# Kernel tuning notes

Hardware: AMD Instinct MI355X
Metric: run time of the kernel (lower is better)

## Reference

```python
import jax, jax.numpy as jnp
import numpy as np

B, S, H, I, E = 2, 2048, 1024, 4096, 8
NUM_STEPS = 2
RMS_EPS = 1e-6


def rmsnorm(x, w, eps=RMS_EPS):
    var = jnp.mean(jnp.square(x), axis=-1, keepdims=True)
    return x * jax.lax.rsqrt(var + eps) * w


def setup_inputs() -> dict:
    key = jax.random.key(0)
    ks = jax.random.split(key, 7)
    return {
        "hidden_states": jax.random.normal(ks[0], (B, S, H), dtype=jnp.float32),
        "gate_w": jax.random.normal(ks[1], (E, H), dtype=jnp.float32) * 0.02,
        "w1": jax.random.normal(ks[2], (E, H, I), dtype=jnp.float32) * 0.02,
        "b1": jnp.zeros((E, I), dtype=jnp.float32),
        "w2": jax.random.normal(ks[3], (E, I, H), dtype=jnp.float32) * 0.02,
        "b2": jnp.zeros((E, H), dtype=jnp.float32),
        "ln_w": jnp.ones((H,), dtype=jnp.float32),
    }


def reference(hidden_states, gate_w, w1, b1, w2, b2, ln_w):
    x = hidden_states  # [B,S,H]
    dtype = hidden_states.dtype
    for i in range(NUM_STEPS):
        inp = x if i == 0 else rmsnorm(x, ln_w)
        t = inp.reshape(-1, H)  # [T,H], T = B*S
        # softmax gate (computed in fp32 as in the original)
        logits = t @ gate_w.T  # [T,E]
        rw = jax.nn.softmax(logits.astype(jnp.float32), axis=-1).astype(dtype)
        # all experts on all tokens (dense MoE), batched over E
        h = jax.nn.silu(jnp.einsum('td,edi->tei', t, w1) + b1)  # [T,E,I]
        eo = jnp.einsum('tei,eih->teh', h, w2) + b2             # [T,E,H]
        comb = jnp.einsum('te,teh->th', rw, eo)                 # weighted combine
        x = x + comb.reshape(B, S, H)
    return x  # final_projection is Identity (no feature extractor)
```

## Files before the change

### kernel.cpp

```cpp
#include <hip/hip_runtime.h>
#include <hip/hip_bf16.h>

#define T_TOK 4096
#define H_DIM 1024
#define I_DIM 4096
#define E_EXP 8
#define RMS_EPS_F 1e-6f

using bf16x8 = __attribute__((ext_vector_type(8))) __bf16;
using f32x4  = __attribute__((ext_vector_type(4))) float;

__device__ inline void gload_lds16(const void* g, void* l) {
    __builtin_amdgcn_global_load_lds(
        (const __attribute__((address_space(1))) void*)g,
        (__attribute__((address_space(3))) void*)l,
        16, 0, 0);
}

__global__ __launch_bounds__(256) void k_transpose_cvt(
    const float* __restrict__ in, __hip_bfloat16* __restrict__ out, int R, int C)
{
    __shared__ float tile[32][33];
    const size_t mat = (size_t)R * C;
    in  += (size_t)blockIdx.z * mat;
    out += (size_t)blockIdx.z * mat;
    const int c0 = blockIdx.x * 32, r0 = blockIdx.y * 32;
    const int tx = threadIdx.x & 31, ty = threadIdx.x >> 5;
#pragma unroll
    for (int dy = 0; dy < 32; dy += 8)
        tile[ty + dy][tx] = in[(size_t)(r0 + ty + dy) * C + (c0 + tx)];
    __syncthreads();
#pragma unroll
    for (int dy = 0; dy < 32; dy += 8)
        out[(size_t)(c0 + ty + dy) * R + (r0 + tx)] = __float2bfloat16(tile[tx][ty + dy]);
}

__global__ __launch_bounds__(256) void k_prep(
    const float* __restrict__ x, const float* __restrict__ lnw,
    __hip_bfloat16* __restrict__ tb, int do_norm)
{
    const int t = blockIdx.x;
    const float* row = x + (size_t)t * H_DIM;
    const int base = threadIdx.x * 4;
    float4 v = *(const float4*)(row + base);
    if (do_norm) {
        float ss = v.x*v.x + v.y*v.y + v.z*v.z + v.w*v.w;
#pragma unroll
        for (int off = 32; off > 0; off >>= 1) ss += __shfl_xor(ss, off);
        __shared__ float wsum[4];
        const int w = threadIdx.x >> 6;
        if ((threadIdx.x & 63) == 0) wsum[w] = ss;
        __syncthreads();
        const float tot = wsum[0] + wsum[1] + wsum[2] + wsum[3];
        const float scale = rsqrtf(tot * (1.0f / H_DIM) + RMS_EPS_F);
        float4 g = *(const float4*)(lnw + base);
        v.x *= scale * g.x; v.y *= scale * g.y; v.z *= scale * g.z; v.w *= scale * g.w;
    }
    __hip_bfloat16* o = tb + (size_t)t * H_DIM + base;
    o[0] = __float2bfloat16(v.x); o[1] = __float2bfloat16(v.y);
    o[2] = __float2bfloat16(v.z); o[3] = __float2bfloat16(v.w);
}

__global__ __launch_bounds__(256) void k_gate(
    const __hip_bfloat16* __restrict__ tb, const float* __restrict__ gw,
    float* __restrict__ rw)
{
    const int t = blockIdx.x * 4 + (threadIdx.x >> 6);
    const int lane = threadIdx.x & 63;
    const __hip_bfloat16* row = tb + (size_t)t * H_DIM;
    float acc[E_EXP];
#pragma unroll
    for (int e = 0; e < E_EXP; ++e) acc[e] = 0.f;
    for (int h = lane; h < H_DIM; h += 64) {
        const float xv = __bfloat162float(row[h]);
#pragma unroll
        for (int e = 0; e < E_EXP; ++e) acc[e] += xv * gw[e * H_DIM + h];
    }
#pragma unroll
    for (int e = 0; e < E_EXP; ++e) {
#pragma unroll
        for (int off = 32; off > 0; off >>= 1) acc[e] += __shfl_xor(acc[e], off);
    }
    if (lane == 0) {
        float mx = acc[0];
#pragma unroll
        for (int e = 1; e < E_EXP; ++e) mx = fmaxf(mx, acc[e]);
        float ex[E_EXP], s = 0.f;
#pragma unroll
        for (int e = 0; e < E_EXP; ++e) { ex[e] = __expf(acc[e] - mx); s += ex[e]; }
        const float inv = 1.f / s;
#pragma unroll
        for (int e = 0; e < E_EXP; ++e) rw[(size_t)t * E_EXP + e] = ex[e] * inv;
    }
}


template<int BB, int MBASE>
__device__ __forceinline__ void ld_a4(bf16x8 (&a)[4], const char* rdA, int kof) {
#pragma unroll
    for (int mi = 0; mi < 4; ++mi)
        a[mi] = *(const bf16x8*)(rdA + BB * 32768 + (MBASE + mi) * 2048 + kof);
}
template<int BB>
__device__ __forceinline__ void ld_b4(bf16x8 (&b)[4], const char* rdB, int kof) {
#pragma unroll
    for (int ni = 0; ni < 4; ++ni)
        b[ni] = *(const bf16x8*)(rdB + BB * 32768 + ni * 2048 + kof);
}
template<int MB>
__device__ __forceinline__ void mfma_cell(const bf16x8 (&a)[4], const bf16x8 (&b)[4],
                                          f32x4 (&acc)[8][4]) {
    __builtin_amdgcn_s_setprio(1);
#pragma unroll
    for (int mi = 0; mi < 4; ++mi)
#pragma unroll
        for (int ni = 0; ni < 4; ++ni)
            acc[MB + mi][ni] = __builtin_amdgcn_mfma_f32_16x16x32_bf16(
                a[mi], b[ni], acc[MB + mi][ni], 0, 0, 0);
    __builtin_amdgcn_s_setprio(0);
}

#define BAR()   __builtin_amdgcn_s_barrier()
#define LGKM0() asm volatile("s_waitcnt lgkmcnt(0)")
#define VMW(n)  asm volatile("s_waitcnt vmcnt(" #n ")" ::: "memory")
#define SCHED0() __builtin_amdgcn_sched_barrier(0)

template <int MODE>
__global__ __launch_bounds__(512, 2) void k_gemm8(
    const __hip_bfloat16* __restrict__ A, int lda, long long strideA,
    const __hip_bfloat16* __restrict__ Bt, int ldb, long long strideB,
    const float* __restrict__ bias, int strideBias,
    void* __restrict__ out, int ldo, long long strideOut, int K)
{
    __shared__ __hip_bfloat16 sA[2][2][128 * 64];
    __shared__ __hip_bfloat16 sB[2][2][128 * 64];

    const int z = blockIdx.z;
    A  += (size_t)z * (size_t)strideA;
    Bt += (size_t)z * (size_t)strideB;

    const int tid  = threadIdx.x;
    const int lane = tid & 63;
    const int wid  = tid >> 6;
    const int wr = wid >> 2, wc = wid & 3;
    const int m0 = blockIdx.y * 256, n0 = blockIdx.x * 256;

    const int sr  = tid >> 3;
    const int skb = ((((tid & 7) * 16) ^ ((sr & 7) << 4)) >> 1);
    const __hip_bfloat16* gA = A  + (size_t)(m0 + sr) * lda + skb;
    const __hip_bfloat16* gB = Bt + (size_t)(n0 + sr) * ldb + skb;
    char* const dA = (char*)&sA[0][0][0] + tid * 16;
    char* const dB = (char*)&sB[0][0][0] + tid * 16;

#define STAGE_A(bb, hh, kt) do { \
    const __hip_bfloat16* s_ = gA + (size_t)(hh) * 128 * lda + (size_t)(kt) * 64; \
    gload_lds16(s_,                     dA + (bb) * 32768 + (hh) * 16384); \
    gload_lds16(s_ + (size_t)64 * lda,  dA + (bb) * 32768 + (hh) * 16384 + 8192); \
} while (0)
#define STAGE_B(bb, hh, kt) do { \
    const __hip_bfloat16* s_ = gB + (size_t)(hh) * 128 * ldb + (size_t)(kt) * 64; \
    gload_lds16(s_,                     dB + (bb) * 32768 + (hh) * 16384); \
    gload_lds16(s_ + (size_t)64 * ldb,  dB + (bb) * 32768 + (hh) * 16384 + 8192); \
} while (0)

    const int fr = lane & 15, kg = lane >> 4;
    const int msk  = (fr & 7) << 4;
    const int kof0 = (kg * 16) ^ msk;
    const int kof1 = (64 + kg * 16) ^ msk;
    const char* rdA = (const char*)&sA[0][wr][0] + fr * 128;
    const char* rdB = (const char*)&sB[0][wc >> 1][0] + (wc & 1) * 8192 + fr * 128;

    f32x4  acc[8][4] = {};
    bf16x8 a[4], a2[4], b[4];

    const int NT = K >> 6;

    STAGE_B(0, 0, 0); STAGE_B(0, 1, 0);
    STAGE_A(0, 0, 0); STAGE_A(0, 1, 0);
    STAGE_B(1, 0, 1); STAGE_B(1, 1, 1);
    VMW(4); BAR(); SCHED0();

    for (int i = 0; i < NT / 2 - 1; ++i) {
        const int t1 = 2 * i + 1;
        ld_a4<0, 0>(a, rdA, kof0);
        ld_b4<0>(b, rdB, kof0);
        STAGE_A(1, 0, t1);
        BAR(); LGKM0();
        mfma_cell<0>(a, b, acc);
        BAR();
        ld_a4<0, 4>(a2, rdA, kof0);
        STAGE_A(1, 1, t1);
        BAR(); LGKM0();
        mfma_cell<4>(a2, b, acc);
        BAR();
        ld_a4<0, 4>(a2, rdA, kof1);
        ld_b4<0>(b, rdB, kof1);
        BAR(); LGKM0();
        mfma_cell<4>(a2, b, acc);
        BAR();
        ld_a4<0, 0>(a, rdA, kof1);
        STAGE_B(0, 0, t1 + 1); STAGE_B(0, 1, t1 + 1);
        BAR(); LGKM0();
        mfma_cell<0>(a, b, acc);
        VMW(4); BAR(); SCHED0();
        ld_a4<1, 0>(a, rdA, kof0);
        ld_b4<1>(b, rdB, kof0);
        STAGE_A(0, 0, t1 + 1);
        BAR(); LGKM0();
        mfma_cell<0>(a, b, acc);
        BAR();
        ld_a4<1, 4>(a2, rdA, kof0);
        STAGE_A(0, 1, t1 + 1);
        BAR(); LGKM0();
        mfma_cell<4>(a2, b, acc);
        BAR();
        ld_a4<1, 4>(a2, rdA, kof1);
        ld_b4<1>(b, rdB, kof1);
        BAR(); LGKM0();
        mfma_cell<4>(a2, b, acc);
        BAR();
        ld_a4<1, 0>(a, rdA, kof1);
        STAGE_B(1, 0, t1 + 2); STAGE_B(1, 1, t1 + 2);
        BAR(); LGKM0();
        mfma_cell<0>(a, b, acc);
        VMW(4); BAR(); SCHED0();
    }
    {
        const int t1 = NT - 1;
        ld_a4<0, 0>(a, rdA, kof0);
        ld_b4<0>(b, rdB, kof0);
        STAGE_A(1, 0, t1);
        BAR(); LGKM0();
        mfma_cell<0>(a, b, acc);
        BAR();
        ld_a4<0, 4>(a2, rdA, kof0);
        STAGE_A(1, 1, t1);
        BAR(); LGKM0();
        mfma_cell<4>(a2, b, acc);
        BAR();
        ld_a4<0, 4>(a2, rdA, kof1);
        ld_b4<0>(b, rdB, kof1);
        BAR(); LGKM0();
        mfma_cell<4>(a2, b, acc);
        BAR();
        ld_a4<0, 0>(a, rdA, kof1);
        BAR(); LGKM0();
        mfma_cell<0>(a, b, acc);
        VMW(0); BAR(); SCHED0();
        ld_a4<1, 0>(a, rdA, kof0);
        ld_b4<1>(b, rdB, kof0);
        BAR(); LGKM0();
        mfma_cell<0>(a, b, acc);
        BAR();
        ld_a4<1, 4>(a2, rdA, kof0);
        BAR(); LGKM0();
        mfma_cell<4>(a2, b, acc);
        BAR();
        ld_a4<1, 4>(a2, rdA, kof1);
        ld_b4<1>(b, rdB, kof1);
        BAR(); LGKM0();
        mfma_cell<4>(a2, b, acc);
        BAR();
        ld_a4<1, 0>(a, rdA, kof1);
        BAR(); LGKM0();
        mfma_cell<0>(a, b, acc);
    }

    const int rB = kg * 4;
    if (MODE == 0) {
        __hip_bfloat16* O = (__hip_bfloat16*)out + (size_t)z * (size_t)strideOut;
        const float* bz = bias + (size_t)z * (size_t)strideBias;
#pragma unroll
        for (int mi = 0; mi < 8; ++mi) {
            const int gm = m0 + wr * 128 + mi * 16 + rB;
#pragma unroll
            for (int ni = 0; ni < 4; ++ni) {
                const int gn = n0 + wc * 64 + ni * 16 + fr;
                const float bv = bz[gn];
#pragma unroll
                for (int j = 0; j < 4; ++j) {
                    float v = acc[mi][ni][j] + bv;
                    v = v / (1.f + __expf(-v));
                    O[(size_t)(gm + j) * ldo + gn] = __float2bfloat16(v);
                }
            }
        }
    } else {
        float* O = (float*)out + (size_t)z * (size_t)strideOut;
#pragma unroll
        for (int mi = 0; mi < 8; ++mi) {
            const int gm = m0 + wr * 128 + mi * 16 + rB;
#pragma unroll
            for (int ni = 0; ni < 4; ++ni) {
                const int gn = n0 + wc * 64 + ni * 16 + fr;
#pragma unroll
                for (int j = 0; j < 4; ++j)
                    O[(size_t)(gm + j) * ldo + gn] = acc[mi][ni][j];
            }
        }
    }
#undef STAGE_A
#undef STAGE_B
}

__global__ __launch_bounds__(256) void k_combine(
    const float* __restrict__ eo, const float* __restrict__ rw,
    const float* __restrict__ b2, float* __restrict__ x, int e0, int g)
{
    const int t = blockIdx.x;
    const int h = threadIdx.x * 4;
    float4 acc = *(const float4*)(x + (size_t)t * H_DIM + h);
    for (int j = 0; j < g; ++j) {
        const float w = rw[(size_t)t * E_EXP + e0 + j];
        const float4 v  = *(const float4*)(eo + ((size_t)j * T_TOK + t) * H_DIM + h);
        const float4 bz = *(const float4*)(b2 + (size_t)(e0 + j) * H_DIM + h);
        acc.x += w * (v.x + bz.x);
        acc.y += w * (v.y + bz.y);
        acc.z += w * (v.z + bz.z);
        acc.w += w * (v.w + bz.w);
    }
    *(float4*)(x + (size_t)t * H_DIM + h) = acc;
}

extern "C" void kernel_launch(void* const* d_in, const int* in_sizes, int n_in,
                              void* d_out, int out_size, void* d_ws, size_t ws_size,
                              hipStream_t stream)
{
    const float* hidden = (const float*)d_in[0];
    const float* gate_w = (const float*)d_in[1];
    const float* w1     = (const float*)d_in[2];
    const float* b1     = (const float*)d_in[3];
    const float* w2     = (const float*)d_in[4];
    const float* b2     = (const float*)d_in[5];
    const float* ln_w   = (const float*)d_in[6];
    float* x = (float*)d_out;

    const size_t w1t_b = (size_t)E_EXP * I_DIM * H_DIM * 2;
    const size_t w2t_b = (size_t)E_EXP * H_DIM * I_DIM * 2;
    const size_t tb_b  = (size_t)T_TOK * H_DIM * 2;
    const size_t rw_b  = (size_t)T_TOK * E_EXP * 4;
    const size_t hb1_b = (size_t)T_TOK * I_DIM * 2;
    const size_t eo1_b = (size_t)T_TOK * H_DIM * 4;
    const size_t base_b = w1t_b + w2t_b + tb_b + rw_b;

    int g = 0;
    for (int cand = 8; cand >= 1; cand >>= 1)
        if (base_b + (size_t)cand * (hb1_b + eo1_b) <= ws_size) { g = cand; break; }

    char* ws = (char*)d_ws;
    __hip_bfloat16* w1t = (__hip_bfloat16*)ws;  ws += w1t_b;
    __hip_bfloat16* w2t = (__hip_bfloat16*)ws;  ws += w2t_b;
    __hip_bfloat16* tb  = (__hip_bfloat16*)ws;  ws += tb_b;
    float*          rw  = (float*)ws;           ws += rw_b;
    __hip_bfloat16* hb  = (__hip_bfloat16*)ws;
    float*          eo  = (float*)(ws + (size_t)(g > 0 ? g : 1) * hb1_b);

    hipMemcpyAsync(x, hidden, (size_t)T_TOK * H_DIM * 4, hipMemcpyDeviceToDevice, stream);

    if (g == 0) return;

    k_transpose_cvt<<<dim3(I_DIM / 32, H_DIM / 32, E_EXP), 256, 0, stream>>>(w1, w1t, H_DIM, I_DIM);
    k_transpose_cvt<<<dim3(H_DIM / 32, I_DIM / 32, E_EXP), 256, 0, stream>>>(w2, w2t, I_DIM, H_DIM);

    for (int step = 0; step < 2; ++step) {
        k_prep<<<T_TOK, 256, 0, stream>>>(x, ln_w, tb, step);
        k_gate<<<T_TOK / 4, 256, 0, stream>>>(tb, gate_w, rw);

        for (int e0 = 0; e0 < E_EXP; e0 += g) {
            k_gemm8<0><<<dim3(I_DIM / 256, T_TOK / 256, g), 512, 0, stream>>>(
                tb, H_DIM, 0,
                w1t + (size_t)e0 * I_DIM * H_DIM, H_DIM, (long long)I_DIM * H_DIM,
                b1 + (size_t)e0 * I_DIM, I_DIM,
                hb, I_DIM, (long long)T_TOK * I_DIM, H_DIM);
            k_gemm8<2><<<dim3(H_DIM / 256, T_TOK / 256, g), 512, 0, stream>>>(
                hb, I_DIM, (long long)T_TOK * I_DIM,
                w2t + (size_t)e0 * H_DIM * I_DIM, I_DIM, (long long)H_DIM * I_DIM,
                nullptr, 0,
                eo, H_DIM, (long long)T_TOK * H_DIM, I_DIM);
            k_combine<<<T_TOK, 256, 0, stream>>>(eo, rw, b2, x, e0, g);
        }
    }
}
```

Before: 1.496 ms.

## Restructure GEMM main loop with fewer barriers and fold routing weights into first GEMM

Rewrites the GEMM K-loop as a macro pipeline that issues the next LDS fragment loads ahead of each MFMA block, using extra register buffers and removing most per-step barriers. The routing weight is multiplied into the SiLU output of the first GEMM, so the second GEMM output is already weighted and can be stored as bf16, halving the eo traffic that the combine kernel reads. This trades more register pressure and possible LDS hazards from fewer barriers, plus bf16 rounding of the expert outputs, for less synchronisation and memory traffic.

```diff
diff --git a/kernel.cpp b/kernel.cpp
--- a/kernel.cpp
+++ b/kernel.cpp
@@ -121,7 +121,7 @@
 }
 
 #define BAR()   __builtin_amdgcn_s_barrier()
-#define LGKM0() asm volatile("s_waitcnt lgkmcnt(0)")
+#define LGKM0() asm volatile("s_waitcnt lgkmcnt(0)" ::: "memory")
 #define VMW(n)  asm volatile("s_waitcnt vmcnt(" #n ")" ::: "memory")
 #define SCHED0() __builtin_amdgcn_sched_barrier(0)
 
@@ -130,6 +130,7 @@
     const __hip_bfloat16* __restrict__ A, int lda, long long strideA,
     const __hip_bfloat16* __restrict__ Bt, int ldb, long long strideB,
     const float* __restrict__ bias, int strideBias,
+    const float* __restrict__ rw, int e0,
     void* __restrict__ out, int ldo, long long strideOut, int K)
 {
     __shared__ __hip_bfloat16 sA[2][2][128 * 64];
@@ -171,7 +172,7 @@
     const char* rdB = (const char*)&sB[0][wc >> 1][0] + (wc & 1) * 8192 + fr * 128;
 
     f32x4  acc[8][4] = {};
-    bf16x8 a[4], a2[4], b[4];
+    bf16x8 a[4], b[4], a2[4], a2n[4], bn[4];
 
     const int NT = K >> 6;
 
@@ -180,90 +181,79 @@
     STAGE_B(1, 0, 1); STAGE_B(1, 1, 1);
     VMW(4); BAR(); SCHED0();
 
+#define TILE_PIPE(BB, t) do { \
+     \
+    ld_a4<BB, 0>(a, rdA, kof0); \
+    ld_b4<BB>(b, rdB, kof0); \
+    STAGE_A((BB) ^ 1, 0, (t) + 1); \
+    LGKM0(); SCHED0(); \
+    ld_a4<BB, 4>(a2, rdA, kof0);             \
+    SCHED0(); \
+    mfma_cell<0>(a, b, acc); \
+     \
+    STAGE_A((BB) ^ 1, 1, (t) + 1); \
+    LGKM0(); SCHED0(); \
+    ld_a4<BB, 4>(a2n, rdA, kof1);            \
+    ld_b4<BB>(bn, rdB, kof1); \
+    SCHED0(); \
+    mfma_cell<4>(a2, b, acc); \
+    BAR();                                    \
+     \
+    LGKM0(); SCHED0(); \
+    ld_a4<BB, 0>(a, rdA, kof1);              \
+    SCHED0(); \
+    STAGE_B(BB, 0, (t) + 2); \
+    mfma_cell<4>(a2n, bn, acc); \
+     \
+    LGKM0(); SCHED0(); \
+    STAGE_B(BB, 1, (t) + 2); \
+    mfma_cell<0>(a, bn, acc); \
+    VMW(4); BAR(); SCHED0(); \
+} while (0)
+
     for (int i = 0; i < NT / 2 - 1; ++i) {
-        const int t1 = 2 * i + 1;
+        TILE_PIPE(0, 2 * i);
+        TILE_PIPE(1, 2 * i + 1);
+    }
+    {
         ld_a4<0, 0>(a, rdA, kof0);
         ld_b4<0>(b, rdB, kof0);
-        STAGE_A(1, 0, t1);
-        BAR(); LGKM0();
+        STAGE_A(1, 0, NT - 1);
+        LGKM0(); SCHED0();
+        ld_a4<0, 4>(a2, rdA, kof0);
+        SCHED0();
         mfma_cell<0>(a, b, acc);
-        BAR();
-        ld_a4<0, 4>(a2, rdA, kof0);
-        STAGE_A(1, 1, t1);
-        BAR(); LGKM0();
+        STAGE_A(1, 1, NT - 1);
+        LGKM0(); SCHED0();
+        ld_a4<0, 4>(a2n, rdA, kof1);
+        ld_b4<0>(bn, rdB, kof1);
+        SCHED0();
         mfma_cell<4>(a2, b, acc);
         BAR();
-        ld_a4<0, 4>(a2, rdA, kof1);
-        ld_b4<0>(b, rdB, kof1);
-        BAR(); LGKM0();
-        mfma_cell<4>(a2, b, acc);
-        BAR();
+        LGKM0(); SCHED0();
         ld_a4<0, 0>(a, rdA, kof1);
-        STAGE_B(0, 0, t1 + 1); STAGE_B(0, 1, t1 + 1);
-        BAR(); LGKM0();
-        mfma_cell<0>(a, b, acc);
-        VMW(4); BAR(); SCHED0();
-        ld_a4<1, 0>(a, rdA, kof0);
-        ld_b4<1>(b, rdB, kof0);
-        STAGE_A(0, 0, t1 + 1);
-        BAR(); LGKM0();
-        mfma_cell<0>(a, b, acc);
-        BAR();
-        ld_a4<1, 4>(a2, rdA, kof0);
-        STAGE_A(0, 1, t1 + 1);
-        BAR(); LGKM0();
-        mfma_cell<4>(a2, b, acc);
-        BAR();
-        ld_a4<1, 4>(a2, rdA, kof1);
-        ld_b4<1>(b, rdB, kof1);
-        BAR(); LGKM0();
-        mfma_cell<4>(a2, b, acc);
-        BAR();
-        ld_a4<1, 0>(a, rdA, kof1);
-        STAGE_B(1, 0, t1 + 2); STAGE_B(1, 1, t1 + 2);
-        BAR(); LGKM0();
-        mfma_cell<0>(a, b, acc);
-        VMW(4); BAR(); SCHED0();
-    }
-    {
-        const int t1 = NT - 1;
-        ld_a4<0, 0>(a, rdA, kof0);
-        ld_b4<0>(b, rdB, kof0);
-        STAGE_A(1, 0, t1);
-        BAR(); LGKM0();
-        mfma_cell<0>(a, b, acc);
-        BAR();
-        ld_a4<0, 4>(a2, rdA, kof0);
-        STAGE_A(1, 1, t1);
-        BAR(); LGKM0();
-        mfma_cell<4>(a2, b, acc);
-        BAR();
-        ld_a4<0, 4>(a2, rdA, kof1);
-        ld_b4<0>(b, rdB, kof1);
-        BAR(); LGKM0();
-        mfma_cell<4>(a2, b, acc);
-        BAR();
-        ld_a4<0, 0>(a, rdA, kof1);
-        BAR(); LGKM0();
-        mfma_cell<0>(a, b, acc);
+        SCHED0();
+        mfma_cell<4>(a2n, bn, acc);
+        LGKM0(); SCHED0();
+        mfma_cell<0>(a, bn, acc);
         VMW(0); BAR(); SCHED0();
         ld_a4<1, 0>(a, rdA, kof0);
         ld_b4<1>(b, rdB, kof0);
-        BAR(); LGKM0();
+        LGKM0(); SCHED0();
+        ld_a4<1, 4>(a2, rdA, kof0);
+        SCHED0();
         mfma_cell<0>(a, b, acc);
-        BAR();
-        ld_a4<1, 4>(a2, rdA, kof0);
-        BAR(); LGKM0();
+        LGKM0(); SCHED0();
+        ld_a4<1, 4>(a2n, rdA, kof1);
+        ld_b4<1>(bn, rdB, kof1);
+        SCHED0();
         mfma_cell<4>(a2, b, acc);
-        BAR();
-        ld_a4<1, 4>(a2, rdA, kof1);
-        ld_b4<1>(b, rdB, kof1);
-        BAR(); LGKM0();
-        mfma_cell<4>(a2, b, acc);
-        BAR();
+        LGKM0(); SCHED0();
         ld_a4<1, 0>(a, rdA, kof1);
-        BAR(); LGKM0();
-        mfma_cell<0>(a, b, acc);
+        SCHED0();
+        mfma_cell<4>(a2n, bn, acc);
+        LGKM0(); SCHED0();
+        mfma_cell<0>(a, bn, acc);
     }
 
     const int rB = kg * 4;
@@ -274,19 +264,20 @@
         for (int mi = 0; mi < 8; ++mi) {
             const int gm = m0 + wr * 128 + mi * 16 + rB;
 #pragma unroll
-            for (int ni = 0; ni < 4; ++ni) {
-                const int gn = n0 + wc * 64 + ni * 16 + fr;
-                const float bv = bz[gn];
-#pragma unroll
-                for (int j = 0; j < 4; ++j) {
-                    float v = acc[mi][ni][j] + bv;
+            for (int j = 0; j < 4; ++j) {
+                const int row = gm + j;
+                const float rwv = rw[(size_t)row * E_EXP + e0 + z];
+#pragma unroll
+                for (int ni = 0; ni < 4; ++ni) {
+                    const int gn = n0 + wc * 64 + ni * 16 + fr;
+                    float v = acc[mi][ni][j] + bz[gn];
                     v = v / (1.f + __expf(-v));
-                    O[(size_t)(gm + j) * ldo + gn] = __float2bfloat16(v);
+                    O[(size_t)row * ldo + gn] = __float2bfloat16(rwv * v);
                 }
             }
         }
     } else {
-        float* O = (float*)out + (size_t)z * (size_t)strideOut;
+        __hip_bfloat16* O = (__hip_bfloat16*)out + (size_t)z * (size_t)strideOut;
 #pragma unroll
         for (int mi = 0; mi < 8; ++mi) {
             const int gm = m0 + wr * 128 + mi * 16 + rB;
@@ -295,16 +286,17 @@
                 const int gn = n0 + wc * 64 + ni * 16 + fr;
 #pragma unroll
                 for (int j = 0; j < 4; ++j)
-                    O[(size_t)(gm + j) * ldo + gn] = acc[mi][ni][j];
+                    O[(size_t)(gm + j) * ldo + gn] = __float2bfloat16(acc[mi][ni][j]);
             }
         }
     }
 #undef STAGE_A
 #undef STAGE_B
+#undef TILE_PIPE
 }
 
 __global__ __launch_bounds__(256) void k_combine(
-    const float* __restrict__ eo, const float* __restrict__ rw,
+    const __hip_bfloat16* __restrict__ eo, const float* __restrict__ rw,
     const float* __restrict__ b2, float* __restrict__ x, int e0, int g)
 {
     const int t = blockIdx.x;
@@ -312,12 +304,12 @@
     float4 acc = *(const float4*)(x + (size_t)t * H_DIM + h);
     for (int j = 0; j < g; ++j) {
         const float w = rw[(size_t)t * E_EXP + e0 + j];
-        const float4 v  = *(const float4*)(eo + ((size_t)j * T_TOK + t) * H_DIM + h);
+        const __hip_bfloat16* p = eo + ((size_t)j * T_TOK + t) * H_DIM + h;
         const float4 bz = *(const float4*)(b2 + (size_t)(e0 + j) * H_DIM + h);
-        acc.x += w * (v.x + bz.x);
-        acc.y += w * (v.y + bz.y);
-        acc.z += w * (v.z + bz.z);
-        acc.w += w * (v.w + bz.w);
+        acc.x += __bfloat162float(p[0]) + w * bz.x;
+        acc.y += __bfloat162float(p[1]) + w * bz.y;
+        acc.z += __bfloat162float(p[2]) + w * bz.z;
+        acc.w += __bfloat162float(p[3]) + w * bz.w;
     }
     *(float4*)(x + (size_t)t * H_DIM + h) = acc;
 }
@@ -340,7 +332,7 @@
     const size_t tb_b  = (size_t)T_TOK * H_DIM * 2;
     const size_t rw_b  = (size_t)T_TOK * E_EXP * 4;
     const size_t hb1_b = (size_t)T_TOK * I_DIM * 2;
-    const size_t eo1_b = (size_t)T_TOK * H_DIM * 4;
+    const size_t eo1_b = (size_t)T_TOK * H_DIM * 2;
     const size_t base_b = w1t_b + w2t_b + tb_b + rw_b;
 
     int g = 0;
@@ -353,7 +345,7 @@
     __hip_bfloat16* tb  = (__hip_bfloat16*)ws;  ws += tb_b;
     float*          rw  = (float*)ws;           ws += rw_b;
     __hip_bfloat16* hb  = (__hip_bfloat16*)ws;
-    float*          eo  = (float*)(ws + (size_t)(g > 0 ? g : 1) * hb1_b);
+    __hip_bfloat16* eo  = (__hip_bfloat16*)(ws + (size_t)(g > 0 ? g : 1) * hb1_b);
 
     hipMemcpyAsync(x, hidden, (size_t)T_TOK * H_DIM * 4, hipMemcpyDeviceToDevice, stream);
 
@@ -371,11 +363,13 @@
                 tb, H_DIM, 0,
                 w1t + (size_t)e0 * I_DIM * H_DIM, H_DIM, (long long)I_DIM * H_DIM,
                 b1 + (size_t)e0 * I_DIM, I_DIM,
+                rw, e0,
                 hb, I_DIM, (long long)T_TOK * I_DIM, H_DIM);
             k_gemm8<2><<<dim3(H_DIM / 256, T_TOK / 256, g), 512, 0, stream>>>(
                 hb, I_DIM, (long long)T_TOK * I_DIM,
                 w2t + (size_t)e0 * H_DIM * I_DIM, I_DIM, (long long)H_DIM * I_DIM,
                 nullptr, 0,
+                nullptr, 0,
                 eo, H_DIM, (long long)T_TOK * H_DIM, I_DIM);
             k_combine<<<T_TOK, 256, 0, stream>>>(eo, rw, b2, x, e0, g);
         }
```

Measured after the change: 1.430 ms. 1.05x faster.
